# Kernel optimization log

Hardware: AMD Instinct MI355X
Metric: run time of the kernel (lower is better)

The kernel has to match this reference:

```python
import jax, jax.numpy as jnp
import numpy as np

H, E, DFF = 1024, 8, 4096


def setup_inputs() -> dict:
    key = jax.random.key(0)
    ks = jax.random.split(key, 7)
    s = lambda *shape: 1.0 / np.sqrt(shape[-2] if len(shape) > 1 else shape[-1])
    x = jax.random.normal(ks[0], (2, 2048, H), dtype=jnp.float32)
    Wr = jax.random.normal(ks[1], (H, E), dtype=jnp.float32) * (1.0 / np.sqrt(H))
    br = jnp.zeros((E,), dtype=jnp.float32)
    W1 = jax.random.normal(ks[2], (E, H, DFF), dtype=jnp.float32) * (1.0 / np.sqrt(H))
    b1 = jnp.zeros((E, DFF), dtype=jnp.float32)
    W2 = jax.random.normal(ks[3], (E, DFF, H), dtype=jnp.float32) * (1.0 / np.sqrt(DFF))
    b2 = jnp.zeros((E, H), dtype=jnp.float32)
    return {"x": x, "Wr": Wr, "br": br, "W1": W1, "b1": b1, "W2": W2, "b2": b2}


def reference(x, Wr, br, W1, b1, W2, b2):
    B, S, Hd = x.shape
    n_exp = W1.shape[0]
    xt = x.reshape(-1, Hd)                      # (T, H)
    logits = xt @ Wr + br                       # (T, E)
    probs = jax.nn.softmax(logits, axis=-1)
    gate = jnp.max(probs, axis=-1)              # (T,) top-1 gate value
    idx = jnp.argmax(probs, axis=-1)            # (T,) chosen expert
    # dense all-expert FFN, then one-hot combine (vectorized equivalent of per-token loop)
    h1 = jnp.maximum(jnp.einsum('th,ehf->etf', xt, W1) + b1[:, None, :], 0.0)  # (E,T,DFF)
    ye = jnp.einsum('etf,efh->eth', h1, W2) + b2[:, None, :]                   # (E,T,H)
    onehot = jax.nn.one_hot(idx, n_exp, dtype=xt.dtype)                        # (T,E)
    y = jnp.einsum('te,eth->th', onehot, ye) * gate[:, None]                   # (T,H)
    return y.reshape(B, S, Hd)
```

## Files before the change

### kernel.cpp

```cpp
#include <hip/hip_runtime.h>
#include <stdint.h>

typedef unsigned short u16;
typedef __attribute__((ext_vector_type(8))) short s16x8;
typedef __attribute__((ext_vector_type(4))) float f32x4;

#define NEXP 8
#define HD 1024
#define DFF 4096
#define BM 128
#define BN 128
#define BK 64

__device__ __forceinline__ u16 f2bf(float f) {
  union { float f; unsigned u; } c; c.f = f;
  unsigned r = c.u + 0x7fffu + ((c.u >> 16) & 1u);
  return (u16)(r >> 16);
}

__device__ __forceinline__ void gload_lds16(const void* g, const void* l) {
  __builtin_amdgcn_global_load_lds(
      (const __attribute__((address_space(1))) unsigned int*)(uintptr_t)g,
      (__attribute__((address_space(3))) unsigned int*)(unsigned)(uintptr_t)l,
      16, 0, 0);
}

__global__ __launch_bounds__(64) void zero_k(int* counts) {
  if (threadIdx.x < NEXP) counts[threadIdx.x] = 0;
}

template <int K, int N>
__device__ __forceinline__ void convt_tile(const float* __restrict__ W,
    u16* __restrict__ Wt, int idx, u16 (*T)[72]) {
  const int e = idx >> 10;
  const int ti = idx & 1023;
  const int k0 = (ti % (K / 64)) * 64;
  const int n0 = (ti / (K / 64)) * 64;
  const float* src = W + (size_t)e * K * N;
  u16* dst = Wt + (size_t)e * K * N;
  const int t = threadIdx.x;
  const int kk = t >> 4, c4 = (t & 15) * 4;
#pragma unroll
  for (int r = 0; r < 4; ++r) {
    float4 v = *(const float4*)(src + (size_t)(k0 + r * 16 + kk) * N + n0 + c4);
    T[c4 + 0][r * 16 + kk] = f2bf(v.x);
    T[c4 + 1][r * 16 + kk] = f2bf(v.y);
    T[c4 + 2][r * 16 + kk] = f2bf(v.z);
    T[c4 + 3][r * 16 + kk] = f2bf(v.w);
  }
  __syncthreads();
  const int c8 = (t & 7) * 8;
#pragma unroll
  for (int r = 0; r < 2; ++r) {
    int nn = r * 32 + (t >> 3);
    *(s16x8*)(dst + (size_t)(n0 + nn) * K + k0 + c8) = *(const s16x8*)&T[nn][c8];
  }
}

__global__ __launch_bounds__(256) void prep_k(
    const float* __restrict__ x, const float* __restrict__ Wr,
    const float* __restrict__ br, int* __restrict__ counts,
    int* __restrict__ tok_exp, float* __restrict__ tok_gate,
    const float* __restrict__ W1, u16* __restrict__ W1t,
    const float* __restrict__ W2, u16* __restrict__ W2t, int T) {
  __shared__ u16 Tt[64][72];
  const int bid = blockIdx.x;
  const int NBR = T / 4;
  constexpr int NBC1 = (HD / 64) * (DFF / 64) * NEXP;
  if (bid < NBR) {
    const int w = threadIdx.x >> 6, l = threadIdx.x & 63;
    const int t = bid * 4 + w;
    const float4* xr = (const float4*)(x + (size_t)t * HD);
    float acc[NEXP];
#pragma unroll
    for (int j = 0; j < NEXP; ++j) acc[j] = 0.f;
#pragma unroll
    for (int i = 0; i < 4; ++i) {
      float4 v = xr[l + i * 64];
      const int h = (l + i * 64) * 4;
      const float* w0 = Wr + (size_t)h * NEXP;
#pragma unroll
      for (int c = 0; c < 4; ++c) {
        float xv = (c == 0) ? v.x : (c == 1) ? v.y : (c == 2) ? v.z : v.w;
        const float4* wr4 = (const float4*)(w0 + c * NEXP);
        float4 a = wr4[0], b = wr4[1];
        acc[0] += xv * a.x; acc[1] += xv * a.y; acc[2] += xv * a.z; acc[3] += xv * a.w;
        acc[4] += xv * b.x; acc[5] += xv * b.y; acc[6] += xv * b.z; acc[7] += xv * b.w;
      }
    }
#pragma unroll
    for (int j = 0; j < NEXP; ++j)
#pragma unroll
      for (int off = 32; off > 0; off >>= 1) acc[j] += __shfl_xor(acc[j], off);
    if (l == 0) {
      float lg[NEXP];
      float best = acc[0] + br[0]; int bi = 0;
      lg[0] = best;
#pragma unroll
      for (int j = 1; j < NEXP; ++j) {
        lg[j] = acc[j] + br[j];
        if (lg[j] > best) { best = lg[j]; bi = j; }
      }
      float s = 0.f;
#pragma unroll
      for (int j = 0; j < NEXP; ++j) s += expf(lg[j] - best);
      tok_exp[t] = bi;
      tok_gate[t] = 1.0f / s;
      atomicAdd(&counts[bi], 1);
    }
  } else if (bid < NBR + NBC1) {
    convt_tile<HD, DFF>(W1, W1t, bid - NBR, Tt);
  } else {
    convt_tile<DFF, HD>(W2, W2t, bid - NBR - NBC1, Tt);
  }
}

__global__ __launch_bounds__(64) void scan_k(const int* __restrict__ counts,
    int* __restrict__ seg, int* __restrict__ cursor,
    int* __restrict__ ntile, int* __restrict__ tile_e, int* __restrict__ tile_m) {
  if (threadIdx.x == 0) {
    int s = 0, nt = 0;
#pragma unroll
    for (int e = 0; e < NEXP; ++e) {
      seg[e] = s; cursor[e] = s;
      int c = counts[e];
      for (int m = 0; m < c; m += BM) { tile_e[nt] = e; tile_m[nt] = m; ++nt; }
      s += c;
    }
    seg[NEXP] = s;
    ntile[0] = nt;
  }
}

__global__ __launch_bounds__(256) void gather_k(const float* __restrict__ x,
    const int* __restrict__ tok_exp, const float* __restrict__ tok_gate,
    int* __restrict__ cursor, int* __restrict__ perm, float* __restrict__ gatep,
    u16* __restrict__ Xg) {
  const int w = threadIdx.x >> 6, l = threadIdx.x & 63;
  const int t = blockIdx.x * 4 + w;
  int pos = 0;
  if (l == 0) {
    int e = tok_exp[t];
    pos = atomicAdd(&cursor[e], 1);
    perm[pos] = t;
    gatep[pos] = tok_gate[t];
  }
  pos = __shfl(pos, 0);
  const float4* xr = (const float4*)(x + (size_t)t * HD);
  ushort4* dst = (ushort4*)(Xg + (size_t)pos * HD);
#pragma unroll
  for (int i = 0; i < HD / 4 / 64; ++i) {
    float4 v = xr[l + i * 64];
    ushort4 o;
    o.x = f2bf(v.x); o.y = f2bf(v.y); o.z = f2bf(v.z); o.w = f2bf(v.w);
    dst[l + i * 64] = o;
  }
}

template <int KD, int ND, int EPI, int KSPLIT>
__global__ __launch_bounds__(256, 4) void ffn_gemm(
    const u16* __restrict__ A, const u16* __restrict__ Bt,
    const float* __restrict__ bias, const int* __restrict__ seg,
    const int* __restrict__ ntile, const int* __restrict__ tile_e,
    const int* __restrict__ tile_m,
    u16* __restrict__ H1out, float* __restrict__ Pt) {
  const int bx = blockIdx.x, by = blockIdx.y;
  if (by >= ntile[0]) return;
  const int e  = tile_e[by];
  const int m0 = tile_m[by];
  const int ks = blockIdx.z;
  const int s0 = seg[e];
  const int cnt = seg[e + 1] - s0;
  const int n0 = bx * BN;
  constexpr int NT = (KD / KSPLIT) / BK;
  const int kbase = ks * (KD / KSPLIT);

  __shared__ __align__(16) u16 As[BM * BK];
  __shared__ __align__(16) u16 Bs[BN * BK];

  const int t = threadIdx.x;
  const int l = t & 63, w = t >> 6;
  const int wr = w >> 1, wc = w & 1;

  const f32x4 fzero = {0.f, 0.f, 0.f, 0.f};
  f32x4 acc[4][4];
#pragma unroll
  for (int i = 0; i < 4; ++i)
#pragma unroll
    for (int j = 0; j < 4; ++j) acc[i][j] = fzero;

  const int sub = t & 7, r8 = t >> 3;
  const int koff = (sub ^ (r8 & 7)) * 8;
  int aoff[4], boff[4];
  const u16* bte = Bt + (size_t)e * ND * KD;
#pragma unroll
  for (int c = 0; c < 4; ++c) {
    int row = c * 32 + r8;
    int rg = m0 + row; if (rg >= cnt) rg = cnt - 1;
    aoff[c] = (s0 + rg) * KD + kbase + koff;
    boff[c] = (n0 + row) * KD + kbase + koff;
  }

  for (int tt = 0; tt < NT; ++tt) {
    __syncthreads();
    const int ko = tt * BK;
#pragma unroll
    for (int c = 0; c < 4; ++c)
      gload_lds16(A + (size_t)aoff[c] + ko, &As[(c * 256 + t) * 8]);
#pragma unroll
    for (int c = 0; c < 4; ++c)
      gload_lds16(bte + (size_t)boff[c] + ko, &Bs[(c * 256 + t) * 8]);
    __syncthreads();
#pragma unroll
    for (int s = 0; s < 2; ++s) {
      const int fo = ((s * 4 + (l >> 4)) ^ (l & 7)) * 8;
      s16x8 af[4], bfr[4];
#pragma unroll
      for (int mi = 0; mi < 4; ++mi)
        af[mi] = *(const s16x8*)&As[(wr * 64 + mi * 16 + (l & 15)) * BK + fo];
#pragma unroll
      for (int ni = 0; ni < 4; ++ni)
        bfr[ni] = *(const s16x8*)&Bs[(wc * 64 + ni * 16 + (l & 15)) * BK + fo];
#pragma unroll
      for (int mi = 0; mi < 4; ++mi)
#pragma unroll
        for (int ni = 0; ni < 4; ++ni)
          acc[mi][ni] = __builtin_amdgcn_mfma_f32_16x16x32_bf16(af[mi], bfr[ni], acc[mi][ni], 0, 0, 0);
    }
  }

  const int lr = (l >> 4) * 4;
  const int lc = l & 15;

  if constexpr (EPI == 0) {
    float bv2[4];
#pragma unroll
    for (int ni = 0; ni < 4; ++ni)
      bv2[ni] = bias[(size_t)e * ND + n0 + wc * 64 + ni * 16 + lc];
#pragma unroll
    for (int mi = 0; mi < 4; ++mi) {
#pragma unroll
      for (int r = 0; r < 4; ++r) {
        int row = m0 + wr * 64 + mi * 16 + lr + r;
        if (row < cnt) {
          u16* hrow = H1out + (size_t)(s0 + row) * ND + n0 + wc * 64;
#pragma unroll
          for (int ni = 0; ni < 4; ++ni) {
            float v = acc[mi][ni][r] + bv2[ni];
            v = v > 0.f ? v : 0.f;
            hrow[ni * 16 + lc] = f2bf(v);
          }
        }
      }
    }
  } else {
    const int totT = seg[NEXP];
#pragma unroll
    for (int mi = 0; mi < 4; ++mi) {
#pragma unroll
      for (int r = 0; r < 4; ++r) {
        int row = m0 + wr * 64 + mi * 16 + lr + r;
        if (row < cnt) {
          float* prow = Pt + ((size_t)ks * totT + s0 + row) * ND + n0 + wc * 64;
#pragma unroll
          for (int ni = 0; ni < 4; ++ni)
            prow[ni * 16 + lc] = acc[mi][ni][r];
        }
      }
    }
  }
}

__global__ __launch_bounds__(256) void reduce_k(const float* __restrict__ Pt,
    const float* __restrict__ b2, const int* __restrict__ perm,
    const float* __restrict__ gatep, const int* __restrict__ tok_exp,
    float* __restrict__ out) {
  const int pos = blockIdx.x;
  const int totT = gridDim.x;
  const int tok = perm[pos];
  const float g = gatep[pos];
  const int e = tok_exp[tok];
  const int h = threadIdx.x * 4;
  float4 s = *(const float4*)(Pt + ((size_t)0 * totT + pos) * HD + h);
#pragma unroll
  for (int k = 1; k < 4; ++k) {
    float4 p = *(const float4*)(Pt + ((size_t)k * totT + pos) * HD + h);
    s.x += p.x; s.y += p.y; s.z += p.z; s.w += p.w;
  }
  float4 b = *(const float4*)(b2 + (size_t)e * HD + h);
  float4 o;
  o.x = (s.x + b.x) * g; o.y = (s.y + b.y) * g;
  o.z = (s.z + b.z) * g; o.w = (s.w + b.w) * g;
  *(float4*)(out + (size_t)tok * HD + h) = o;
}

extern "C" void kernel_launch(void* const* d_in, const int* in_sizes, int n_in,
                              void* d_out, int out_size, void* d_ws, size_t ws_size,
                              hipStream_t stream) {
  const float* x  = (const float*)d_in[0];
  const float* Wr = (const float*)d_in[1];
  const float* br = (const float*)d_in[2];
  const float* W1 = (const float*)d_in[3];
  const float* b1 = (const float*)d_in[4];
  const float* W2 = (const float*)d_in[5];
  const float* b2 = (const float*)d_in[6];
  float* out = (float*)d_out;

  const int T = in_sizes[0] / HD;
  char* ws = (char*)d_ws;
  int*   counts   = (int*)(ws + 0);
  int*   cursor   = (int*)(ws + 64);
  int*   seg      = (int*)(ws + 128);
  int*   ntile    = (int*)(ws + 192);
  int*   tile_e   = (int*)(ws + 256);
  int*   tile_m   = (int*)(ws + 512);
  int*   tok_exp  = (int*)(ws + 1024);
  float* tok_gate = (float*)(ws + 1024 + 4 * (size_t)T);
  int*   perm     = (int*)(ws + 1024 + 8 * (size_t)T);
  float* gatep    = (float*)(ws + 1024 + 12 * (size_t)T);
  u16*   Xg       = (u16*)(ws + 1024 + 16 * (size_t)T);
  u16*   H1       = (u16*)(ws + 1024 + 16 * (size_t)T + 2 * (size_t)T * HD);
  size_t off2     = 1024 + 16 * (size_t)T + 2 * (size_t)T * HD + 2 * (size_t)T * DFF;
  u16*   W1t      = (u16*)(ws + off2);
  u16*   W2t      = (u16*)(ws + off2 + 2 * (size_t)NEXP * HD * DFF);
  float* Pt       = (float*)W1t;

  hipLaunchKernelGGL(zero_k, dim3(1), dim3(64), 0, stream, counts);
  const int NBR = T / 4;
  const int NBC = (HD / 64) * (DFF / 64) * NEXP;
  hipLaunchKernelGGL(prep_k, dim3(NBR + 2 * NBC), dim3(256), 0, stream,
                     x, Wr, br, counts, tok_exp, tok_gate, W1, W1t, W2, W2t, T);
  hipLaunchKernelGGL(scan_k, dim3(1), dim3(64), 0, stream, counts, seg, cursor, ntile, tile_e, tile_m);
  hipLaunchKernelGGL(gather_k, dim3(T / 4), dim3(256), 0, stream,
                     x, tok_exp, tok_gate, cursor, perm, gatep, Xg);
  const int maxtile = (T + BM - 1) / BM + NEXP - 1;
  hipLaunchKernelGGL((ffn_gemm<HD, DFF, 0, 1>), dim3(DFF / BN, maxtile, 1), dim3(256), 0, stream,
                     Xg, W1t, b1, seg, ntile, tile_e, tile_m, H1, nullptr);
  hipLaunchKernelGGL((ffn_gemm<DFF, HD, 2, 4>), dim3(HD / BN, maxtile, 4), dim3(256), 0, stream,
                     H1, W2t, nullptr, seg, ntile, tile_e, tile_m, nullptr, Pt);
  hipLaunchKernelGGL(reduce_k, dim3(T), dim3(256), 0, stream, Pt, b2, perm, gatep, tok_exp, out);
}
```

Baseline: 308.6 us.

## Overlap W2 bf16 transpose with first expert GEMM and widen conversion tiles

```diff
diff --git a/kernel.cpp b/kernel.cpp
--- a/kernel.cpp
+++ b/kernel.cpp
@@ -4,6 +4,7 @@
 typedef unsigned short u16;
 typedef __attribute__((ext_vector_type(8))) short s16x8;
 typedef __attribute__((ext_vector_type(4))) float f32x4;
+typedef __attribute__((ext_vector_type(4))) unsigned uint4v;
 
 #define NEXP 8
 #define HD 1024
@@ -12,10 +13,18 @@
 #define BN 128
 #define BK 64
 
+#define CT_S 136
+
 __device__ __forceinline__ u16 f2bf(float f) {
   union { float f; unsigned u; } c; c.f = f;
   unsigned r = c.u + 0x7fffu + ((c.u >> 16) & 1u);
   return (u16)(r >> 16);
+}
+
+__device__ __forceinline__ unsigned cvtpk(float a, float b) {
+  unsigned r;
+  asm("v_cvt_pk_bf16_f32 %0, %1, %2" : "=v"(r) : "v"(a), "v"(b));
+  return r;
 }
 
 __device__ __forceinline__ void gload_lds16(const void* g, const void* l) {
@@ -31,87 +40,90 @@
 
 template <int K, int N>
 __device__ __forceinline__ void convt_tile(const float* __restrict__ W,
-    u16* __restrict__ Wt, int idx, u16 (*T)[72]) {
-  const int e = idx >> 10;
-  const int ti = idx & 1023;
-  const int k0 = (ti % (K / 64)) * 64;
-  const int n0 = (ti / (K / 64)) * 64;
+    u16* __restrict__ Wt, int idx, u16* __restrict__ T) {
+  const int e = idx >> 9;
+  const int ti = idx & 511;
+  const int k0 = (ti % (K / 128)) * 128;
+  const int n0 = (ti / (K / 128)) * 64;
   const float* src = W + (size_t)e * K * N;
   u16* dst = Wt + (size_t)e * K * N;
   const int t = threadIdx.x;
-  const int kk = t >> 4, c4 = (t & 15) * 4;
+  const int m = t & 15, g = t >> 4;
+  const int kq = g * 8, nq = m * 4;
+  f32x4 v[8];
+#pragma unroll
+  for (int i = 0; i < 8; ++i)
+    v[i] = *(const f32x4*)(src + (size_t)(k0 + kq + i) * N + n0 + nq);
+#pragma unroll
+  for (int j = 0; j < 4; ++j) {
+    uint4v q;
+    q[0] = cvtpk(v[0][j], v[1][j]);
+    q[1] = cvtpk(v[2][j], v[3][j]);
+    q[2] = cvtpk(v[4][j], v[5][j]);
+    q[3] = cvtpk(v[6][j], v[7][j]);
+    *(uint4v*)&T[(nq + j) * CT_S + kq] = q;
+  }
+  __syncthreads();
 #pragma unroll
   for (int r = 0; r < 4; ++r) {
-    float4 v = *(const float4*)(src + (size_t)(k0 + r * 16 + kk) * N + n0 + c4);
-    T[c4 + 0][r * 16 + kk] = f2bf(v.x);
-    T[c4 + 1][r * 16 + kk] = f2bf(v.y);
-    T[c4 + 2][r * 16 + kk] = f2bf(v.z);
-    T[c4 + 3][r * 16 + kk] = f2bf(v.w);
-  }
-  __syncthreads();
-  const int c8 = (t & 7) * 8;
-#pragma unroll
-  for (int r = 0; r < 2; ++r) {
-    int nn = r * 32 + (t >> 3);
-    *(s16x8*)(dst + (size_t)(n0 + nn) * K + k0 + c8) = *(const s16x8*)&T[nn][c8];
-  }
-}
-
-__global__ __launch_bounds__(256) void prep_k(
+    const int nn = r * 16 + g;
+    const int c8 = m * 8;
+    uint4v q = *(const uint4v*)&T[nn * CT_S + c8];
+    *(uint4v*)(dst + (size_t)(n0 + nn) * K + k0 + c8) = q;
+  }
+}
+
+__global__ __launch_bounds__(256) void prep1_k(
     const float* __restrict__ x, const float* __restrict__ Wr,
     const float* __restrict__ br, int* __restrict__ counts,
     int* __restrict__ tok_exp, float* __restrict__ tok_gate,
-    const float* __restrict__ W1, u16* __restrict__ W1t,
-    const float* __restrict__ W2, u16* __restrict__ W2t, int T) {
-  __shared__ u16 Tt[64][72];
+    const float* __restrict__ W1, u16* __restrict__ W1t, int T) {
+  __shared__ __align__(16) u16 Tt[64 * CT_S];
   const int bid = blockIdx.x;
   const int NBR = T / 4;
-  constexpr int NBC1 = (HD / 64) * (DFF / 64) * NEXP;
-  if (bid < NBR) {
-    const int w = threadIdx.x >> 6, l = threadIdx.x & 63;
-    const int t = bid * 4 + w;
-    const float4* xr = (const float4*)(x + (size_t)t * HD);
-    float acc[NEXP];
-#pragma unroll
-    for (int j = 0; j < NEXP; ++j) acc[j] = 0.f;
-#pragma unroll
-    for (int i = 0; i < 4; ++i) {
-      float4 v = xr[l + i * 64];
-      const int h = (l + i * 64) * 4;
-      const float* w0 = Wr + (size_t)h * NEXP;
-#pragma unroll
-      for (int c = 0; c < 4; ++c) {
-        float xv = (c == 0) ? v.x : (c == 1) ? v.y : (c == 2) ? v.z : v.w;
-        const float4* wr4 = (const float4*)(w0 + c * NEXP);
-        float4 a = wr4[0], b = wr4[1];
-        acc[0] += xv * a.x; acc[1] += xv * a.y; acc[2] += xv * a.z; acc[3] += xv * a.w;
-        acc[4] += xv * b.x; acc[5] += xv * b.y; acc[6] += xv * b.z; acc[7] += xv * b.w;
-      }
-    }
-#pragma unroll
-    for (int j = 0; j < NEXP; ++j)
-#pragma unroll
-      for (int off = 32; off > 0; off >>= 1) acc[j] += __shfl_xor(acc[j], off);
-    if (l == 0) {
-      float lg[NEXP];
-      float best = acc[0] + br[0]; int bi = 0;
-      lg[0] = best;
-#pragma unroll
-      for (int j = 1; j < NEXP; ++j) {
-        lg[j] = acc[j] + br[j];
-        if (lg[j] > best) { best = lg[j]; bi = j; }
-      }
-      float s = 0.f;
-#pragma unroll
-      for (int j = 0; j < NEXP; ++j) s += expf(lg[j] - best);
-      tok_exp[t] = bi;
-      tok_gate[t] = 1.0f / s;
-      atomicAdd(&counts[bi], 1);
-    }
-  } else if (bid < NBR + NBC1) {
+  if (bid >= NBR) {
     convt_tile<HD, DFF>(W1, W1t, bid - NBR, Tt);
-  } else {
-    convt_tile<DFF, HD>(W2, W2t, bid - NBR - NBC1, Tt);
+    return;
+  }
+  const int w = threadIdx.x >> 6, l = threadIdx.x & 63;
+  const int t = bid * 4 + w;
+  const float4* xr = (const float4*)(x + (size_t)t * HD);
+  float acc[NEXP];
+#pragma unroll
+  for (int j = 0; j < NEXP; ++j) acc[j] = 0.f;
+#pragma unroll
+  for (int i = 0; i < 4; ++i) {
+    float4 v = xr[l + i * 64];
+    const int h = (l + i * 64) * 4;
+    const float* w0 = Wr + (size_t)h * NEXP;
+#pragma unroll
+    for (int c = 0; c < 4; ++c) {
+      float xv = (c == 0) ? v.x : (c == 1) ? v.y : (c == 2) ? v.z : v.w;
+      const float4* wr4 = (const float4*)(w0 + c * NEXP);
+      float4 a = wr4[0], b = wr4[1];
+      acc[0] += xv * a.x; acc[1] += xv * a.y; acc[2] += xv * a.z; acc[3] += xv * a.w;
+      acc[4] += xv * b.x; acc[5] += xv * b.y; acc[6] += xv * b.z; acc[7] += xv * b.w;
+    }
+  }
+#pragma unroll
+  for (int j = 0; j < NEXP; ++j)
+#pragma unroll
+    for (int off = 32; off > 0; off >>= 1) acc[j] += __shfl_xor(acc[j], off);
+  if (l == 0) {
+    float lg[NEXP];
+    float best = acc[0] + br[0]; int bi = 0;
+    lg[0] = best;
+#pragma unroll
+    for (int j = 1; j < NEXP; ++j) {
+      lg[j] = acc[j] + br[j];
+      if (lg[j] > best) { best = lg[j]; bi = j; }
+    }
+    float s = 0.f;
+#pragma unroll
+    for (int j = 0; j < NEXP; ++j) s += expf(lg[j] - best);
+    tok_exp[t] = bi;
+    tok_gate[t] = 1.0f / s;
+    atomicAdd(&counts[bi], 1);
   }
 }
 
@@ -158,25 +170,22 @@
 }
 
 template <int KD, int ND, int EPI, int KSPLIT>
-__global__ __launch_bounds__(256, 4) void ffn_gemm(
+__device__ __forceinline__ void gemm_body(
+    u16* __restrict__ As, u16* __restrict__ Bs,
     const u16* __restrict__ A, const u16* __restrict__ Bt,
     const float* __restrict__ bias, const int* __restrict__ seg,
     const int* __restrict__ ntile, const int* __restrict__ tile_e,
     const int* __restrict__ tile_m,
-    u16* __restrict__ H1out, float* __restrict__ Pt) {
-  const int bx = blockIdx.x, by = blockIdx.y;
+    u16* __restrict__ H1out, float* __restrict__ Pt,
+    int bx, int by, int ks) {
   if (by >= ntile[0]) return;
   const int e  = tile_e[by];
   const int m0 = tile_m[by];
-  const int ks = blockIdx.z;
   const int s0 = seg[e];
   const int cnt = seg[e + 1] - s0;
   const int n0 = bx * BN;
   constexpr int NT = (KD / KSPLIT) / BK;
   const int kbase = ks * (KD / KSPLIT);
-
-  __shared__ __align__(16) u16 As[BM * BK];
-  __shared__ __align__(16) u16 Bs[BN * BK];
 
   const int t = threadIdx.x;
   const int l = t & 63, w = t >> 6;
@@ -269,6 +278,32 @@
       }
     }
   }
+}
+
+__global__ __launch_bounds__(256, 4) void gemm1_fused_k(
+    const u16* __restrict__ Xg, const u16* __restrict__ W1t,
+    const float* __restrict__ b1, const int* __restrict__ seg,
+    const int* __restrict__ ntile, const int* __restrict__ tile_e,
+    const int* __restrict__ tile_m, u16* __restrict__ H1,
+    const float* __restrict__ W2, u16* __restrict__ W2t, int ng1) {
+  __shared__ __align__(16) u16 sh[2 * BM * BK];
+  const int bid = blockIdx.x;
+  if (bid < ng1) {
+    gemm_body<HD, DFF, 0, 1>(sh, sh + BM * BK, Xg, W1t, b1, seg, ntile, tile_e,
+                             tile_m, H1, nullptr, bid % (DFF / BN), bid / (DFF / BN), 0);
+  } else {
+    convt_tile<DFF, HD>(W2, W2t, bid - ng1, sh);
+  }
+}
+
+__global__ __launch_bounds__(256, 4) void gemm2_k(
+    const u16* __restrict__ H1, const u16* __restrict__ W2t,
+    const int* __restrict__ seg, const int* __restrict__ ntile,
+    const int* __restrict__ tile_e, const int* __restrict__ tile_m,
+    float* __restrict__ Pt) {
+  __shared__ __align__(16) u16 sh[2 * BM * BK];
+  gemm_body<DFF, HD, 2, 4>(sh, sh + BM * BK, H1, W2t, nullptr, seg, ntile, tile_e,
+                           tile_m, nullptr, Pt, blockIdx.x, blockIdx.y, blockIdx.z);
 }
 
 __global__ __launch_bounds__(256) void reduce_k(const float* __restrict__ Pt,
@@ -327,16 +362,17 @@
 
   hipLaunchKernelGGL(zero_k, dim3(1), dim3(64), 0, stream, counts);
   const int NBR = T / 4;
-  const int NBC = (HD / 64) * (DFF / 64) * NEXP;
-  hipLaunchKernelGGL(prep_k, dim3(NBR + 2 * NBC), dim3(256), 0, stream,
-                     x, Wr, br, counts, tok_exp, tok_gate, W1, W1t, W2, W2t, T);
+  const int NCT = 512 * NEXP;
+  hipLaunchKernelGGL(prep1_k, dim3(NBR + NCT), dim3(256), 0, stream,
+                     x, Wr, br, counts, tok_exp, tok_gate, W1, W1t, T);
   hipLaunchKernelGGL(scan_k, dim3(1), dim3(64), 0, stream, counts, seg, cursor, ntile, tile_e, tile_m);
   hipLaunchKernelGGL(gather_k, dim3(T / 4), dim3(256), 0, stream,
                      x, tok_exp, tok_gate, cursor, perm, gatep, Xg);
   const int maxtile = (T + BM - 1) / BM + NEXP - 1;
-  hipLaunchKernelGGL((ffn_gemm<HD, DFF, 0, 1>), dim3(DFF / BN, maxtile, 1), dim3(256), 0, stream,
-                     Xg, W1t, b1, seg, ntile, tile_e, tile_m, H1, nullptr);
-  hipLaunchKernelGGL((ffn_gemm<DFF, HD, 2, 4>), dim3(HD / BN, maxtile, 4), dim3(256), 0, stream,
-                     H1, W2t, nullptr, seg, ntile, tile_e, tile_m, nullptr, Pt);
+  const int ng1 = (DFF / BN) * maxtile;
+  hipLaunchKernelGGL(gemm1_fused_k, dim3(ng1 + NCT), dim3(256), 0, stream,
+                     Xg, W1t, b1, seg, ntile, tile_e, tile_m, H1, W2, W2t, ng1);
+  hipLaunchKernelGGL(gemm2_k, dim3(HD / BN, maxtile, 4), dim3(256), 0, stream,
+                     H1, W2t, seg, ntile, tile_e, tile_m, Pt);
   hipLaunchKernelGGL(reduce_k, dim3(T), dim3(256), 0, stream, Pt, b2, perm, gatep, tok_exp, out);
 }
```

Measured after the change: 297.2 us. -3.7%, faster.
